# Kernel tuning notes

Measured on AMD Instinct MI355X. Metric: run time of the kernel, lower is better.

The kernel has to match this reference:

```python
import jax, jax.numpy as jnp
import numpy as np

BETA = 0.9       # snn.Leaky(beta=0.9)
THRESH = 1.0     # snntorch default threshold, reset_mechanism='subtract'


def setup_inputs() -> dict:
    key = jax.random.key(0)
    ks = jax.random.split(key, 7)
    B = 16384
    return {
        "x":  jax.random.normal(ks[0], (B, 1700), dtype=jnp.float32),
        "W1": jax.random.normal(ks[1], (64, 1700), dtype=jnp.float32) * 0.02,
        "b1": jax.random.normal(ks[2], (64,), dtype=jnp.float32) * 0.02,
        "W2": jax.random.normal(ks[3], (32, 64), dtype=jnp.float32) * 0.1,
        "b2": jax.random.normal(ks[4], (32,), dtype=jnp.float32) * 0.1,
        "W3": jax.random.normal(ks[5], (2, 32), dtype=jnp.float32) * 0.1,
        "b3": jax.random.normal(ks[6], (2,), dtype=jnp.float32) * 0.1,
        "num_steps": 20,
    }


def _lif_step(mem, cur):
    # snntorch Leaky: reset (subtract) based on previous mem crossing threshold,
    # then leaky integration of the new input current.
    reset = (mem > THRESH).astype(mem.dtype)
    return BETA * mem + cur - reset * THRESH


def reference(x, W1, b1, W2, b2, W3, b3, num_steps):
    B = x.shape[0]
    # Dropout is identity in eval mode; x is constant across steps, so cur1 is
    # loop-invariant and computed once (same math as the original loop).
    cur1 = x @ W1.T + b1                         # [B, 64]

    def step(carry, _):
        mem1, mem2 = carry
        mem1 = _lif_step(mem1, cur1)             # [B, 64]
        cur2 = mem1 @ W2.T + b2                  # [B, 32]
        mem2 = _lif_step(mem2, cur2)             # [B, 32]
        return (mem1, mem2), None

    init = (jnp.zeros((B, 64), x.dtype), jnp.zeros((B, 32), x.dtype))
    (mem1, mem2), _ = jax.lax.scan(step, init, None, length=num_steps)
    return mem2 @ W3.T + b3                      # [B, 2]
```

## Files before the change

### kernel.cpp

```cpp
#include <hip/hip_runtime.h>
#include <hip/hip_bf16.h>

typedef float f32x4 __attribute__((ext_vector_type(4)));
typedef short bf16x8 __attribute__((ext_vector_type(8)));
typedef _Float16 f16x8 __attribute__((ext_vector_type(8)));

#define MFMA16  __builtin_amdgcn_mfma_f32_16x16x32_bf16
#define MFMA16F __builtin_amdgcn_mfma_f32_16x16x32_f16

static constexpr int KDIM = 1700;
static constexpr int NKT2 = 56;
static constexpr float BETA = 0.9f;
static constexpr float THRESH = 1.0f;

__device__ __forceinline__ void split_bf(float f, short& hi, short& lo) {
    __hip_bfloat16 h = __float2bfloat16(f);
    float r = f - __bfloat162float(h);
    __hip_bfloat16 l = __float2bfloat16(r);
    hi = (short)__builtin_bit_cast(unsigned short, h);
    lo = (short)__builtin_bit_cast(unsigned short, l);
}

__device__ __forceinline__ void split8(f32x4 a, f32x4 b, bf16x8& hi, bf16x8& lo) {
    #pragma unroll
    for (int i = 0; i < 4; ++i) { short h, l; split_bf(a[i], h, l); hi[i] = h; lo[i] = l; }
    #pragma unroll
    for (int i = 0; i < 4; ++i) { short h, l; split_bf(b[i], h, l); hi[4 + i] = h; lo[4 + i] = l; }
}

__device__ __forceinline__ void split8h(f32x4 a, f32x4 b, f16x8& hi, f16x8& lo) {
    #pragma unroll
    for (int i = 0; i < 4; ++i) {
        _Float16 h = (_Float16)a[i];
        hi[i] = h; lo[i] = (_Float16)(a[i] - (float)h);
    }
    #pragma unroll
    for (int i = 0; i < 4; ++i) {
        _Float16 h = (_Float16)b[i];
        hi[4 + i] = h; lo[4 + i] = (_Float16)(b[i] - (float)h);
    }
}

__global__ void w1_relayout(const float* __restrict__ W1, _Float16* __restrict__ WT) {
    const int g    = blockIdx.x * 256 + threadIdx.x;
    const int kt   = g >> 8;
    const int nt   = (g >> 6) & 3;
    const int lane = g & 63;
    const int n    = nt * 16 + (lane & 15);
    const int kb   = kt * 32 + (lane >> 4) * 8;
    f16x8 v;
    #pragma unroll
    for (int i = 0; i < 8; ++i) {
        const int k = kb + i;
        v[i] = (k < KDIM) ? (_Float16)W1[n * KDIM + k] : (_Float16)0.f;
    }
    *(f16x8*)(WT + (size_t)g * 8) = v;
}

__device__ __forceinline__ void gll16(const void* src, const void* lds_dst) {
    __builtin_amdgcn_global_load_lds(
        (const __attribute__((address_space(1))) unsigned int*)src,
        (__attribute__((address_space(3))) unsigned int*)lds_dst, 16, 0, 0);
}

__global__ __launch_bounds__(256, 2) void snn_fused(
    const float* __restrict__ x, const _Float16* __restrict__ WT,
    const float* __restrict__ b1, const float* __restrict__ W2,
    const float* __restrict__ b2, const float* __restrict__ W3,
    const float* __restrict__ b3, const int* __restrict__ nsp,
    float* __restrict__ out)
{
    __shared__ __align__(16) char smemraw[65536];
    _Float16* ldsW = (_Float16*)smemraw;
    float (*red)[32][68] = (float (*)[32][68])smemraw;

    const int tid = threadIdx.x;
    const int wid = tid >> 6;
    const int lane = tid & 63;
    const int l15 = lane & 15;
    const int g4  = lane >> 4;
    const int kg  = g4 * 8;
    const int rowBase = blockIdx.x * 32;
    const int t0  = wid * 14;

    const float* xr0 = x + (size_t)(rowBase + l15) * KDIM;
    const float* xr1 = xr0 + (size_t)16 * KDIM;
    const _Float16* pW = WT + (size_t)t0 * 2048 + lane * 8;
    _Float16* myLds = ldsW + wid * 8192;

    struct XB { f32x4 a0, a1, b0, b1; };
    auto xload = [&](int t, XB& xb) {
        const int k1 = t * 32 + kg;
        const int kc1 = (k1 <= 1696) ? k1 : 1664;
        const int kc2 = (k1 + 4 <= 1696) ? k1 + 4 : 1664;
        const float* p0 = xr0 + kc1;
        const float* p1 = xr0 + kc2;
        const float* p2 = xr1 + kc1;
        const float* p3 = xr1 + kc2;
        asm volatile("global_load_dwordx4 %0, %1, off" : "=v"(xb.a0) : "v"(p0));
        asm volatile("global_load_dwordx4 %0, %1, off" : "=v"(xb.a1) : "v"(p1));
        asm volatile("global_load_dwordx4 %0, %1, off" : "=v"(xb.b0) : "v"(p2));
        asm volatile("global_load_dwordx4 %0, %1, off" : "=v"(xb.b1) : "v"(p3));
    };
    auto stageW = [&](int i, int buf) {
        _Float16* dstb = myLds + buf * 2048;
        #pragma unroll
        for (int q = 0; q < 4; ++q)
            gll16(pW + (size_t)i * 2048 + q * 512, dstb + q * 512);
    };

    f32x4 acc[2][4] = {};
    XB x0, x1, x2, x3, x4;

    stageW(0, 0); xload(t0 + 0, x0);
    stageW(1, 1); xload(t0 + 1, x1);
    stageW(2, 2); xload(t0 + 2, x2);
    stageW(3, 3); xload(t0 + 3, x3);
    xload(t0 + 4, x4);

#define GSTEP(I, XC, WAITN)                                                    \
    {                                                                          \
        asm volatile("s_waitcnt vmcnt(" #WAITN ")" ::: "memory");              \
        __builtin_amdgcn_sched_barrier(0);                                     \
        const _Float16* rb = myLds + ((I) & 3) * 2048;                         \
        f16x8 WC[4];                                                           \
        _Pragma("unroll")                                                      \
        for (int q = 0; q < 4; ++q)                                            \
            WC[q] = *(const f16x8*)(rb + q * 512 + lane * 8);                  \
        f16x8 ah0, al0, ah1, al1;                                              \
        split8h(XC.a0, XC.a1, ah0, al0);                                       \
        split8h(XC.b0, XC.b1, ah1, al1);                                       \
        asm volatile("s_waitcnt lgkmcnt(0)" ::: "memory");                     \
        __builtin_amdgcn_sched_barrier(0);                                     \
        if constexpr ((I) + 4 < 14) stageW((I) + 4, (I) & 3);                  \
        if constexpr ((I) + 5 < 14) xload(t0 + (I) + 5, XC);                   \
        __builtin_amdgcn_sched_barrier(0);                                     \
        _Pragma("unroll")                                                      \
        for (int nt = 0; nt < 4; ++nt) {                                       \
            acc[0][nt] = MFMA16F(ah0, WC[nt], acc[0][nt], 0, 0, 0);            \
            acc[0][nt] = MFMA16F(al0, WC[nt], acc[0][nt], 0, 0, 0);            \
            acc[1][nt] = MFMA16F(ah1, WC[nt], acc[1][nt], 0, 0, 0);            \
            acc[1][nt] = MFMA16F(al1, WC[nt], acc[1][nt], 0, 0, 0);            \
        }                                                                      \
    }

    GSTEP(0,  x0, 28)
    GSTEP(1,  x1, 28)
    GSTEP(2,  x2, 28)
    GSTEP(3,  x3, 28)
    GSTEP(4,  x4, 28)
    GSTEP(5,  x0, 28)
    GSTEP(6,  x1, 28)
    GSTEP(7,  x2, 28)
    GSTEP(8,  x3, 28)
    GSTEP(9,  x4, 28)
    GSTEP(10, x0, 24)
    GSTEP(11, x1, 16)
    GSTEP(12, x2, 8)
    GSTEP(13, x3, 0)
#undef GSTEP

    __syncthreads();

    #pragma unroll
    for (int mt = 0; mt < 2; ++mt)
        #pragma unroll
        for (int nt = 0; nt < 4; ++nt)
            #pragma unroll
            for (int j = 0; j < 4; ++j)
                red[wid][mt * 16 + g4 * 4 + j][nt * 16 + l15] = acc[mt][nt][j];
    __syncthreads();

    {
        const int rr  = tid >> 3;
        const int seg = tid & 7;
        f32x4 s0 = *(const f32x4*)(b1 + seg * 8);
        f32x4 s1 = *(const f32x4*)(b1 + seg * 8 + 4);
        #pragma unroll
        for (int p = 0; p < 4; ++p) {
            s0 += *(const f32x4*)&red[p][rr][seg * 8];
            s1 += *(const f32x4*)&red[p][rr][seg * 8 + 4];
        }
        *(f32x4*)&red[0][rr][seg * 8]     = s0;
        *(f32x4*)&red[0][rr][seg * 8 + 4] = s1;
    }
    __syncthreads();
    if (wid >= 2) return;

    const int lrow = wid * 16 + l15;

    float c1[2][8], c1m1[2][8];
    #pragma unroll
    for (int kt = 0; kt < 2; ++kt) {
        f32x4 u0 = *(const f32x4*)&red[0][lrow][kt * 32 + kg];
        f32x4 u1 = *(const f32x4*)&red[0][lrow][kt * 32 + kg + 4];
        #pragma unroll
        for (int i = 0; i < 4; ++i) {
            c1[kt][i] = u0[i];     c1[kt][4 + i] = u1[i];
            c1m1[kt][i] = u0[i] - THRESH; c1m1[kt][4 + i] = u1[i] - THRESH;
        }
    }

    bf16x8 W2hf[2][2], W2lf[2][2];
    #pragma unroll
    for (int rt = 0; rt < 2; ++rt)
        #pragma unroll
        for (int kt = 0; kt < 2; ++kt) {
            const float* wp = W2 + (rt * 16 + l15) * 64 + kt * 32 + kg;
            split8(*(const f32x4*)wp, *(const f32x4*)(wp + 4), W2hf[rt][kt], W2lf[rt][kt]);
        }

    float b2v[2][4], b2m1[2][4], w3a[2][4], w3b[2][4];
    #pragma unroll
    for (int nt = 0; nt < 2; ++nt)
        #pragma unroll
        for (int j = 0; j < 4; ++j) {
            const int o = nt * 16 + g4 * 4 + j;
            b2v[nt][j]  = b2[o];
            b2m1[nt][j] = b2[o] - THRESH;
            w3a[nt][j] = W3[o];
            w3b[nt][j] = W3[32 + o];
        }

    float m1[2][8] = {};
    float m2[2][4] = {};
    const int ns = nsp[0];
    for (int s = 0; s < ns; ++s) {
        bf16x8 mh[2], ml[2];
        #pragma unroll
        for (int kt = 0; kt < 2; ++kt)
            #pragma unroll
            for (int i = 0; i < 8; ++i) {
                float m = m1[kt][i];
                m = __builtin_fmaf(BETA, m, (m > THRESH) ? c1m1[kt][i] : c1[kt][i]);
                m1[kt][i] = m;
                short h, l; split_bf(m, h, l);
                mh[kt][i] = h; ml[kt][i] = l;
            }
        f32x4 a2[2][2] = {};
        #pragma unroll
        for (int rt = 0; rt < 2; ++rt)
            #pragma unroll
            for (int kt = 0; kt < 2; ++kt) {
                a2[rt][kt] = MFMA16(W2hf[rt][kt], mh[kt], a2[rt][kt], 0, 0, 0);
                a2[rt][kt] = MFMA16(W2lf[rt][kt], mh[kt], a2[rt][kt], 0, 0, 0);
                a2[rt][kt] = MFMA16(W2hf[rt][kt], ml[kt], a2[rt][kt], 0, 0, 0);
            }
        #pragma unroll
        for (int nt = 0; nt < 2; ++nt) {
            f32x4 c2 = a2[nt][0] + a2[nt][1];
            #pragma unroll
            for (int j = 0; j < 4; ++j) {
                float m = m2[nt][j];
                m2[nt][j] = __builtin_fmaf(
                    BETA, m, c2[j] + ((m > THRESH) ? b2m1[nt][j] : b2v[nt][j]));
            }
        }
    }

    float p0 = 0.f, p1 = 0.f;
    #pragma unroll
    for (int nt = 0; nt < 2; ++nt)
        #pragma unroll
        for (int j = 0; j < 4; ++j) {
            p0 = __builtin_fmaf(m2[nt][j], w3a[nt][j], p0);
            p1 = __builtin_fmaf(m2[nt][j], w3b[nt][j], p1);
        }
    p0 += __shfl_xor(p0, 16); p0 += __shfl_xor(p0, 32);
    p1 += __shfl_xor(p1, 16); p1 += __shfl_xor(p1, 32);
    if (lane < 16) {
        const size_t row = rowBase + lrow;
        out[row * 2 + 0] = p0 + b3[0];
        out[row * 2 + 1] = p1 + b3[1];
    }
}

extern "C" void kernel_launch(void* const* d_in, const int* in_sizes, int n_in,
                              void* d_out, int out_size, void* d_ws, size_t ws_size,
                              hipStream_t stream) {
    const float* x  = (const float*)d_in[0];
    const float* W1 = (const float*)d_in[1];
    const float* b1 = (const float*)d_in[2];
    const float* W2 = (const float*)d_in[3];
    const float* b2 = (const float*)d_in[4];
    const float* W3 = (const float*)d_in[5];
    const float* b3 = (const float*)d_in[6];
    const int*   ns = (const int*)d_in[7];
    float* o = (float*)d_out;

    const int B = in_sizes[0] / KDIM;
    _Float16* WT = (_Float16*)d_ws;

    w1_relayout<<<NKT2, 256, 0, stream>>>(W1, WT);
    snn_fused<<<B / 32, 256, 0, stream>>>(x, WT, b1, W2, b2, W3, b3, ns, o);
}
```

Before: 41.09 us.

## Process two K-tiles per pipeline step with double-buffered W and x prefetch

Restructures the GEMM main loop so each step consumes two 32-wide K tiles: W staging writes 8 chunks into one of two 4096-element LDS buffers, and x loads 8 vectors for two tiles at once. This replaces the 4-deep W ring and 5-deep x ring with 2-deep buffering at doubled granularity. The goal is fewer waits and barriers per unit of work and larger MFMA bursts between them. In exchange, prefetch runs less far ahead and register use rises (8 W fragments, 8 x vectors per buffer).

Result: no change. 41.02 us (-0.2%).

```diff
diff --git a/kernel.cpp b/kernel.cpp
--- a/kernel.cpp
+++ b/kernel.cpp
@@ -88,52 +88,55 @@
     const _Float16* pW = WT + (size_t)t0 * 2048 + lane * 8;
     _Float16* myLds = ldsW + wid * 8192;
 
-    struct XB { f32x4 a0, a1, b0, b1; };
-    auto xload = [&](int t, XB& xb) {
-        const int k1 = t * 32 + kg;
-        const int kc1 = (k1 <= 1696) ? k1 : 1664;
-        const int kc2 = (k1 + 4 <= 1696) ? k1 + 4 : 1664;
-        const float* p0 = xr0 + kc1;
-        const float* p1 = xr0 + kc2;
-        const float* p2 = xr1 + kc1;
-        const float* p3 = xr1 + kc2;
-        asm volatile("global_load_dwordx4 %0, %1, off" : "=v"(xb.a0) : "v"(p0));
-        asm volatile("global_load_dwordx4 %0, %1, off" : "=v"(xb.a1) : "v"(p1));
-        asm volatile("global_load_dwordx4 %0, %1, off" : "=v"(xb.b0) : "v"(p2));
-        asm volatile("global_load_dwordx4 %0, %1, off" : "=v"(xb.b1) : "v"(p3));
+    struct XB2 { f32x4 v[8]; };
+    auto xload2 = [&](int d, XB2& xb) {
+        #pragma unroll
+        for (int j = 0; j < 2; ++j) {
+            const int t  = t0 + 2 * d + j;
+            const int k1 = t * 32 + kg;
+            const int kc1 = (k1 <= 1696) ? k1 : 1664;
+            const int kc2 = (k1 + 4 <= 1696) ? k1 + 4 : 1664;
+            const float* p0 = xr0 + kc1;
+            const float* p1 = xr0 + kc2;
+            const float* p2 = xr1 + kc1;
+            const float* p3 = xr1 + kc2;
+            asm volatile("global_load_dwordx4 %0, %1, off" : "=v"(xb.v[4*j+0]) : "v"(p0));
+            asm volatile("global_load_dwordx4 %0, %1, off" : "=v"(xb.v[4*j+1]) : "v"(p1));
+            asm volatile("global_load_dwordx4 %0, %1, off" : "=v"(xb.v[4*j+2]) : "v"(p2));
+            asm volatile("global_load_dwordx4 %0, %1, off" : "=v"(xb.v[4*j+3]) : "v"(p3));
+        }
     };
-    auto stageW = [&](int i, int buf) {
-        _Float16* dstb = myLds + buf * 2048;
-        #pragma unroll
-        for (int q = 0; q < 4; ++q)
-            gll16(pW + (size_t)i * 2048 + q * 512, dstb + q * 512);
+    auto stageW2 = [&](int d, int buf) {
+        _Float16* dstb = myLds + buf * 4096;
+        #pragma unroll
+        for (int q = 0; q < 8; ++q)
+            gll16(pW + (size_t)(2 * d) * 2048 + q * 512, dstb + q * 512);
     };
 
     f32x4 acc[2][4] = {};
-    XB x0, x1, x2, x3, x4;
-
-    stageW(0, 0); xload(t0 + 0, x0);
-    stageW(1, 1); xload(t0 + 1, x1);
-    stageW(2, 2); xload(t0 + 2, x2);
-    stageW(3, 3); xload(t0 + 3, x3);
-    xload(t0 + 4, x4);
-
-#define GSTEP(I, XC, WAITN)                                                    \
+    XB2 x0, x1;
+
+    stageW2(0, 0); xload2(0, x0);
+    stageW2(1, 1); xload2(1, x1);
+
+#define GSTEP2(I, XC, WAITN)                                                   \
     {                                                                          \
         asm volatile("s_waitcnt vmcnt(" #WAITN ")" ::: "memory");              \
         __builtin_amdgcn_sched_barrier(0);                                     \
-        const _Float16* rb = myLds + ((I) & 3) * 2048;                         \
-        f16x8 WC[4];                                                           \
+        const _Float16* rb = myLds + ((I) & 1) * 4096;                         \
+        f16x8 WC[8];                                                           \
         _Pragma("unroll")                                                      \
-        for (int q = 0; q < 4; ++q)                                            \
+        for (int q = 0; q < 8; ++q)                                            \
             WC[q] = *(const f16x8*)(rb + q * 512 + lane * 8);                  \
-        f16x8 ah0, al0, ah1, al1;                                              \
-        split8h(XC.a0, XC.a1, ah0, al0);                                       \
-        split8h(XC.b0, XC.b1, ah1, al1);                                       \
+        f16x8 ah0, al0, ah1, al1, ch0, cl0, ch1, cl1;                          \
+        split8h(XC.v[0], XC.v[1], ah0, al0);                                   \
+        split8h(XC.v[2], XC.v[3], ah1, al1);                                   \
+        split8h(XC.v[4], XC.v[5], ch0, cl0);                                   \
+        split8h(XC.v[6], XC.v[7], ch1, cl1);                                   \
         asm volatile("s_waitcnt lgkmcnt(0)" ::: "memory");                     \
         __builtin_amdgcn_sched_barrier(0);                                     \
-        if constexpr ((I) + 4 < 14) stageW((I) + 4, (I) & 3);                  \
-        if constexpr ((I) + 5 < 14) xload(t0 + (I) + 5, XC);                   \
+        if constexpr ((I) + 2 < 7) { stageW2((I) + 2, (I) & 1);                \
+                                     xload2((I) + 2, XC); }                    \
         __builtin_amdgcn_sched_barrier(0);                                     \
         _Pragma("unroll")                                                      \
         for (int nt = 0; nt < 4; ++nt) {                                       \
@@ -142,23 +145,23 @@
             acc[1][nt] = MFMA16F(ah1, WC[nt], acc[1][nt], 0, 0, 0);            \
             acc[1][nt] = MFMA16F(al1, WC[nt], acc[1][nt], 0, 0, 0);            \
         }                                                                      \
-    }
-
-    GSTEP(0,  x0, 28)
-    GSTEP(1,  x1, 28)
-    GSTEP(2,  x2, 28)
-    GSTEP(3,  x3, 28)
-    GSTEP(4,  x4, 28)
-    GSTEP(5,  x0, 28)
-    GSTEP(6,  x1, 28)
-    GSTEP(7,  x2, 28)
-    GSTEP(8,  x3, 28)
-    GSTEP(9,  x4, 28)
-    GSTEP(10, x0, 24)
-    GSTEP(11, x1, 16)
-    GSTEP(12, x2, 8)
-    GSTEP(13, x3, 0)
-#undef GSTEP
+        _Pragma("unroll")                                                      \
+        for (int nt = 0; nt < 4; ++nt) {                                       \
+            acc[0][nt] = MFMA16F(ch0, WC[4 + nt], acc[0][nt], 0, 0, 0);        \
+            acc[0][nt] = MFMA16F(cl0, WC[4 + nt], acc[0][nt], 0, 0, 0);        \
+            acc[1][nt] = MFMA16F(ch1, WC[4 + nt], acc[1][nt], 0, 0, 0);        \
+            acc[1][nt] = MFMA16F(cl1, WC[4 + nt], acc[1][nt], 0, 0, 0);        \
+        }                                                                      \
+    }
+
+    GSTEP2(0, x0, 16)
+    GSTEP2(1, x1, 16)
+    GSTEP2(2, x0, 16)
+    GSTEP2(3, x1, 16)
+    GSTEP2(4, x0, 16)
+    GSTEP2(5, x1, 16)
+    GSTEP2(6, x0, 0)
+#undef GSTEP2
 
     __syncthreads();
 
```
